# Kernel optimization log

Measured on AMD Instinct MI355X. Metric: run time of the kernel, lower is better.

## Reference

```python
import jax, jax.numpy as jnp
import numpy as np
import math

FEAT_DIM = 256
QUERY_DIM = 256
HIDDEN = 64
OUT_DIM = 256
HEADS = 8


def setup_inputs() -> dict:
    key = jax.random.key(0)
    ks = jax.random.split(key, 10)
    B, NQ, NKV = 2, 2048, 2048
    s_q = 1.0 / math.sqrt(QUERY_DIM)
    s_f = 1.0 / math.sqrt(FEAT_DIM)
    s_o = 1.0 / math.sqrt(HIDDEN * HEADS)
    return {
        "feat": jax.random.normal(ks[0], (B, NKV, FEAT_DIM), jnp.float32),
        "query": jax.random.normal(ks[1], (B, NQ, QUERY_DIM), jnp.float32),
        # stacked per-head weights (each head has its own Linear in torch)
        "Wq": jax.random.uniform(ks[2], (HEADS, QUERY_DIM, HIDDEN), jnp.float32, -s_q, s_q),
        "bq": jax.random.uniform(ks[3], (HEADS, HIDDEN), jnp.float32, -s_q, s_q),
        "Wk": jax.random.uniform(ks[4], (HEADS, FEAT_DIM, HIDDEN), jnp.float32, -s_f, s_f),
        "bk": jax.random.uniform(ks[5], (HEADS, HIDDEN), jnp.float32, -s_f, s_f),
        "Wv": jax.random.uniform(ks[6], (HEADS, FEAT_DIM, HIDDEN), jnp.float32, -s_f, s_f),
        "bv": jax.random.uniform(ks[7], (HEADS, HIDDEN), jnp.float32, -s_f, s_f),
        "Wo": jax.random.uniform(ks[8], (HEADS * HIDDEN, OUT_DIM), jnp.float32, -s_o, s_o),
        "bo": jax.random.uniform(ks[9], (OUT_DIM,), jnp.float32, -s_o, s_o),
    }


def reference(feat, query, Wq, bq, Wk, bk, Wv, bv, Wo, bo):
    # Per-head projections, vectorized over the head axis h.
    # q: [B, H, Nq, E]; k, v: [B, H, Nkv, E]
    q = jnp.einsum("bnd,hde->bhne", query, Wq) + bq[None, :, None, :]
    k = jnp.einsum("bnd,hde->bhne", feat, Wk) + bk[None, :, None, :]
    v = jnp.einsum("bnd,hde->bhne", feat, Wv) + bv[None, :, None, :]
    scale = 1.0 / math.sqrt(HIDDEN)
    scores = jnp.einsum("bhqe,bhke->bhqk", q, k) * scale  # [B, H, Nq, Nkv]
    prob = jax.nn.softmax(scores, axis=-1)
    # dropout p=0.0 (eval) -> identity
    heads = jnp.einsum("bhqk,bhke->bhqe", prob, v)  # [B, H, Nq, E]
    # concat heads in order (head 0 first) then output projection
    B, H, NQ, E = heads.shape
    cat = heads.transpose(0, 2, 1, 3).reshape(B, NQ, H * E)
    return cat @ Wo + bo
```

## Files before the change

kernel.cpp:

```cpp
#include <hip/hip_runtime.h>
#include <hip/hip_bf16.h>

typedef unsigned short u16;
typedef __attribute__((ext_vector_type(8))) short short8;
typedef __attribute__((ext_vector_type(4))) float f32x4;
typedef __attribute__((ext_vector_type(16))) float f32x16;
typedef __attribute__((ext_vector_type(2))) int v2i;

#define HEADS 8
#define HID 64
#define QSCALE 0.18033688011112042f

__device__ inline u16 f2bf(float f){
    unsigned u = __float_as_uint(f);
    unsigned r = (u + 0x7fffu + ((u >> 16) & 1u)) >> 16;
    return (u16)r;
}

__device__ inline int cvtpk(float lo, float hi){
    int r;
    asm("v_cvt_pk_bf16_f32 %0, %1, %2" : "=v"(r) : "v"(lo), "v"(hi));
    return r;
}

__device__ inline float exp2fast(float x){
    float r;
    asm("v_exp_f32 %0, %1" : "=v"(r) : "v"(x));
    return r;
}

__device__ inline float xhalf_sum(float x){
    v2i r = __builtin_amdgcn_permlane32_swap(__float_as_int(x), __float_as_int(x), false, false);
    return __int_as_float(r.x) + __int_as_float(r.y);
}

__global__ __launch_bounds__(256) void prep_weights(
    const float* __restrict__ query, const float* __restrict__ feat,
    const float* __restrict__ Wq, const float* __restrict__ Wk,
    const float* __restrict__ Wv, const float* __restrict__ Wo,
    u16* __restrict__ Xbq, u16* __restrict__ Xbf,
    u16* __restrict__ WfT, u16* __restrict__ WoT)
{
    int id = blockIdx.x * 256 + threadIdx.x;
    if (id < 262144) {
        const float* src = (id < 131072) ? query : feat;
        u16* dst = (id < 131072) ? Xbq : Xbf;
        int r = (id < 131072) ? id : id - 131072;
        int row = r >> 5;
        int rb = row >> 5, r5 = row & 31;
        int ks = (r & 31) >> 1, hi = r & 1;
        float4 a = *reinterpret_cast<const float4*>(&src[r * 8]);
        float4 b = *reinterpret_cast<const float4*>(&src[r * 8 + 4]);
        uint4 s;
        s.x = (unsigned)cvtpk(a.x, a.y);
        s.y = (unsigned)cvtpk(a.z, a.w);
        s.z = (unsigned)cvtpk(b.x, b.y);
        s.w = (unsigned)cvtpk(b.z, b.w);
        *reinterpret_cast<uint4*>(&dst[((rb * 16 + ks) * 64 + hi * 32 + r5) * 8]) = s;
    } else if (id < 655360) {
        int id2 = id - 262144;
        int w = id2 / 131072;
        int r = id2 % 131072;
        int c = r >> 8;
        int d = r & 255;
        const float* W = (w == 0) ? Wq : (w == 1 ? Wk : Wv);
        size_t idx = (size_t)(((w * 16 + (c >> 5)) * 16 + (d >> 4)) * 64
                              + ((d >> 3) & 1) * 32 + (c & 31)) * 8 + (d & 7);
        WfT[idx] = f2bf(W[(c >> 6) * (256 * 64) + d * 64 + (c & 63)]);
    } else {
        int r = id - 655360;
        int o = r >> 9;
        int k = r & 511;
        WoT[o * 512 + k] = f2bf(Wo[k * 256 + o]);
    }
}

__global__ __launch_bounds__(256, 2) void proj_kernel(
    const u16* __restrict__ Xbq, const u16* __restrict__ Xbf,
    const u16* __restrict__ WfT,
    const float* __restrict__ bq, const float* __restrict__ bk, const float* __restrict__ bv,
    u16* __restrict__ Qb, u16* __restrict__ KVf)
{
    int lb = blockIdx.x;
    int which = lb % 3;
    int rem = lb / 3;
    int rb = rem & 127;
    int nh = rem >> 7;
    const u16* Xb = (which == 0) ? Xbq : Xbf;
    const float* bias = (which == 0) ? bq : (which == 1 ? bk : bv);

    int t = threadIdx.x, lane = t & 63, w = t >> 6;
    int l31 = lane & 31, hh = lane >> 5;

    __shared__ __align__(16) u16 Xl[8192];

    {
        const u16* gsrc = Xb + (size_t)rb * 8192;
        #pragma unroll
        for (int c = 0; c < 4; c++) {
            int off = (w * 4 + c) * 512 + lane * 8;
            __builtin_amdgcn_global_load_lds(
                (const __attribute__((address_space(1))) unsigned int*)(const void*)(gsrc + off),
                (__attribute__((address_space(3))) unsigned int*)(void*)(Xl + off),
                16, 0, 0);
        }
    }
    asm volatile("s_waitcnt vmcnt(0)" ::: "memory");
    __syncthreads();

    int nb0 = nh * 8 + w * 2;
    const u16* W0 = WfT + (size_t)(which * 16 + nb0) * 8192 + lane * 8;
    const u16* W1 = W0 + 8192;

    f32x16 acc0 = {}, acc1 = {};
    #pragma unroll
    for (int ks = 0; ks < 16; ks++) {
        short8 xf = *reinterpret_cast<const short8*>(Xl + ks * 512 + lane * 8);
        short8 w0 = *reinterpret_cast<const short8*>(W0 + ks * 512);
        short8 w1 = *reinterpret_cast<const short8*>(W1 + ks * 512);
        if (which == 2) {
            acc0 = __builtin_amdgcn_mfma_f32_32x32x16_bf16(xf, w0, acc0, 0, 0, 0);
            acc1 = __builtin_amdgcn_mfma_f32_32x32x16_bf16(xf, w1, acc1, 0, 0, 0);
        } else {
            acc0 = __builtin_amdgcn_mfma_f32_32x32x16_bf16(w0, xf, acc0, 0, 0, 0);
            acc1 = __builtin_amdgcn_mfma_f32_32x32x16_bf16(w1, xf, acc1, 0, 0, 0);
        }
    }

    int h = nh * 4 + w;
    int nbase = nh * 256 + w * 64;

    if (which != 2) {
        int m = rb * 32 + l31;
        int b_ = m >> 11, nq = m & 2047;
        int bh = b_ * 8 + h;
        int tile = nq >> 6, nl = nq & 63;
        #pragma unroll
        for (int f = 0; f < 2; f++) {
            const f32x16& A = f ? acc1 : acc0;
            #pragma unroll
            for (int g = 0; g < 4; g++) {
                int e0 = f * 32 + g * 8 + 4 * hh;
                float4 b4 = *reinterpret_cast<const float4*>(&bias[nbase + e0]);
                float v0 = A[4*g+0] + b4.x, v1 = A[4*g+1] + b4.y;
                float v2 = A[4*g+2] + b4.z, v3 = A[4*g+3] + b4.w;
                v2i st;
                if (which == 0) {
                    st.x = cvtpk(v0 * QSCALE, v1 * QSCALE);
                    st.y = cvtpk(v2 * QSCALE, v3 * QSCALE);
                    *reinterpret_cast<v2i*>(&Qb[(size_t)(bh * 2048 + nq) * 64 + e0]) = st;
                } else {
                    st.x = cvtpk(v0, v1);
                    st.y = cvtpk(v2, v3);
                    int regK = ((nl >> 5) << 2) | (e0 >> 4);
                    int lnK  = (nl & 31) | (((e0 >> 3) & 1) << 5);
                    size_t idx = (size_t)(bh * 32 + tile) * 8192 + regK * 512 + lnK * 8 + (e0 & 7);
                    *reinterpret_cast<v2i*>(&KVf[idx]) = st;
                }
            }
        }
    } else {
        #pragma unroll
        for (int f = 0; f < 2; f++) {
            const f32x16& A = f ? acc1 : acc0;
            int n_g = nbase + f * 32 + l31;
            int e = n_g & 63;
            float bscal = bias[n_g];
            #pragma unroll
            for (int g = 0; g < 4; g++) {
                int kvl = g * 8 + 4 * hh;
                int m = rb * 32 + kvl;
                int b_ = m >> 11, nkv = m & 2047;
                int tile = nkv >> 6, nl = nkv & 63;
                int bh = b_ * 8 + h;
                float v0 = A[4*g+0] + bscal, v1 = A[4*g+1] + bscal;
                float v2 = A[4*g+2] + bscal, v3 = A[4*g+3] + bscal;
                v2i st;
                st.x = cvtpk(v0, v1);
                st.y = cvtpk(v2, v3);
                int regV = ((e >> 5) << 2) | (nl >> 4);
                int lnV  = (e & 31) | (((nl >> 3) & 1) << 5);
                size_t idx = (size_t)(bh * 32 + tile) * 8192 + 4096 + regV * 512 + lnV * 8 + (nl & 7);
                *reinterpret_cast<v2i*>(&KVf[idx]) = st;
            }
        }
    }
}

__global__ __launch_bounds__(512, 2) void attn_kernel(
    const u16* __restrict__ Qb, const u16* __restrict__ KVf, u16* __restrict__ cat)
{
    int lb = blockIdx.x;
    int chunk = lb >> 4;
    int bh = ((lb & 7) << 1) | ((lb >> 3) & 1);
    int b_ = bh >> 3, head = bh & 7;
    int t = threadIdx.x, lane = t & 63, w = t >> 6;
    int l31 = lane & 31, hh = lane >> 5;
    int sp = w >> 1, kvh = w & 1, wi = w >> 1;
    int q0 = chunk * 128 + sp * 32;

    __shared__ __align__(16) u16 smem[34304];
    u16* tiles = smem;
    float* Ol = (float*)smem;
    float* Ll = (float*)((char*)smem + 67584);

    const u16* KVfB = KVf + ((size_t)(bh * 32 + kvh * 16)) * 8192;

    short8 qf[4];
    {
        const u16* qp = Qb + (bh * 2048 + q0 + l31) * 64 + hh * 8;
        #pragma unroll
        for (int kc = 0; kc < 4; kc++)
            qf[kc] = *reinterpret_cast<const short8*>(qp + kc * 16);
    }
    asm volatile("s_waitcnt vmcnt(0)" ::: "memory");

#define PACKP(sb, base, out) {                                              \
        int A0 = cvtpk(sb[base+0], sb[base+1]);                             \
        int B0 = cvtpk(sb[base+4], sb[base+5]);                             \
        v2i r0 = __builtin_amdgcn_permlane32_swap(A0, B0, false, false);    \
        int A1 = cvtpk(sb[base+2], sb[base+3]);                             \
        int B1 = cvtpk(sb[base+6], sb[base+7]);                             \
        v2i r1 = __builtin_amdgcn_permlane32_swap(A1, B1, false, false);    \
        union { int i[4]; short8 s; } uu;                                   \
        uu.i[0] = r0.x; uu.i[1] = r1.x; uu.i[2] = r0.y; uu.i[3] = r1.y;     \
        out = uu.s; }

    auto stage = [&](int buf, int tile) {
        const u16* gsrc = KVfB + (size_t)tile * 8192;
        u16* ldst = tiles + (kvh * 2 + buf) * 8192;
        #pragma unroll
        for (int c = 0; c < 4; c++) {
            int off = (wi * 4 + c) * 512 + lane * 8;
            __builtin_amdgcn_global_load_lds(
                (const __attribute__((address_space(1))) unsigned int*)(const void*)(gsrc + off),
                (__attribute__((address_space(3))) unsigned int*)(void*)(ldst + off),
                16, 0, 0);
        }
    };

    f32x16 o0 = {}, o1 = {};
    float ac0 = 0.f, ac1 = 0.f, ac2 = 0.f, ac3 = 0.f;

    stage(0, 0);
    int cur = 0;
    for (int tt = 0; tt < 16; tt++) {
        if (tt < 15) {
            stage(cur ^ 1, tt + 1);
            asm volatile("s_waitcnt vmcnt(4)" ::: "memory");
        } else {
            asm volatile("s_waitcnt vmcnt(0)" ::: "memory");
        }
        __builtin_amdgcn_s_barrier();
        __builtin_amdgcn_sched_barrier(0);

        const u16* kbase = tiles + (kvh * 2 + cur) * 8192;
        short8 kf[8], vf[8];
        #pragma unroll
        for (int r = 0; r < 8; r++)
            kf[r] = *reinterpret_cast<const short8*>(kbase + r * 512 + lane * 8);
        #pragma unroll
        for (int r = 0; r < 8; r++)
            vf[r] = *reinterpret_cast<const short8*>(kbase + 4096 + r * 512 + lane * 8);

        f32x16 s0 = {}, s1 = {};
        #pragma unroll
        for (int kc = 0; kc < 4; kc++)
            s0 = __builtin_amdgcn_mfma_f32_32x32x16_bf16(kf[kc], qf[kc], s0, 0, 0, 0);
        #pragma unroll
        for (int kc = 0; kc < 4; kc++)
            s1 = __builtin_amdgcn_mfma_f32_32x32x16_bf16(kf[4 + kc], qf[kc], s1, 0, 0, 0);

        #pragma unroll
        for (int r = 0; r < 16; r++) {
            float p0 = exp2fast(s0[r]);
            float p1 = exp2fast(s1[r]);
            s0[r] = p0; s1[r] = p1;
            if ((r & 3) == 0) ac0 += p0 + p1;
            else if ((r & 3) == 1) ac1 += p0 + p1;
            else if ((r & 3) == 2) ac2 += p0 + p1;
            else ac3 += p0 + p1;
        }

        short8 pf[4];
        PACKP(s0, 0, pf[0]); PACKP(s0, 8, pf[1]);
        PACKP(s1, 0, pf[2]); PACKP(s1, 8, pf[3]);

        #pragma unroll
        for (int c = 0; c < 4; c++) {
            o0 = __builtin_amdgcn_mfma_f32_32x32x16_bf16(vf[c],     pf[c], o0, 0, 0, 0);
            o1 = __builtin_amdgcn_mfma_f32_32x32x16_bf16(vf[4 + c], pf[c], o1, 0, 0, 0);
        }

        asm volatile("s_waitcnt lgkmcnt(0)" ::: "memory");
        __builtin_amdgcn_s_barrier();
        __builtin_amdgcn_sched_barrier(0);
        cur ^= 1;
    }

    float lrun = xhalf_sum((ac0 + ac1) + (ac2 + ac3));

    #pragma unroll
    for (int eb = 0; eb < 2; eb++) {
        #pragma unroll
        for (int r = 0; r < 16; r++) {
            int d = eb * 32 + (r & 3) + 8 * (r >> 2) + 4 * hh;
            Ol[(w * 64 + d) * 33 + l31] = eb ? o1[r] : o0[r];
        }
    }
    if (hh == 0) Ll[w * 32 + l31] = lrun;
    __syncthreads();

    {
        int msp = t >> 7;
        int tt2 = t & 127;
        int q = tt2 >> 2;
        int d0 = (tt2 & 3) * 16;
        int wA = msp * 2, wB = msp * 2 + 1;
        float lsum = Ll[wA * 32 + q] + Ll[wB * 32 + q];
        float linv = 1.0f / lsum;
        float vv[16];
        #pragma unroll
        for (int j = 0; j < 16; j++)
            vv[j] = (Ol[(wA * 64 + d0 + j) * 33 + q] +
                     Ol[(wB * 64 + d0 + j) * 33 + q]) * linv;
        uint4 st0, st1;
        st0.x = (unsigned)cvtpk(vv[0],  vv[1]);
        st0.y = (unsigned)cvtpk(vv[2],  vv[3]);
        st0.z = (unsigned)cvtpk(vv[4],  vv[5]);
        st0.w = (unsigned)cvtpk(vv[6],  vv[7]);
        st1.x = (unsigned)cvtpk(vv[8],  vv[9]);
        st1.y = (unsigned)cvtpk(vv[10], vv[11]);
        st1.z = (unsigned)cvtpk(vv[12], vv[13]);
        st1.w = (unsigned)cvtpk(vv[14], vv[15]);
        u16* crow = cat + (b_ * 2048 + chunk * 128 + msp * 32 + q) * 512 + head * 64 + d0;
        *reinterpret_cast<uint4*>(crow) = st0;
        *reinterpret_cast<uint4*>(crow + 8) = st1;
    }
#undef PACKP
}

__global__ __launch_bounds__(256) void outproj_kernel(
    const u16* __restrict__ cat, const u16* __restrict__ WoT,
    const float* __restrict__ bo, float* __restrict__ out)
{
    int m0 = blockIdx.x * 64, n0 = blockIdx.y * 64;
    int t = threadIdx.x, lane = t & 63, w = t >> 6;
    int l15 = lane & 15, kof = (lane >> 4) * 8;

    __shared__ __align__(16) u16 lA[64][72];
    __shared__ __align__(16) u16 lB[64][72];

    f32x4 acc[4] = {};
    for (int kt = 0; kt < 512; kt += 64) {
        #pragma unroll
        for (int i = 0; i < 2; i++) {
            int lin = t + i * 256;
            int row = lin >> 3, c8 = (lin & 7) * 8;
            *reinterpret_cast<uint4*>(&lA[row][c8]) =
                *reinterpret_cast<const uint4*>(&cat[(m0 + row) * 512 + kt + c8]);
            *reinterpret_cast<uint4*>(&lB[row][c8]) =
                *reinterpret_cast<const uint4*>(&WoT[(n0 + row) * 512 + kt + c8]);
        }
        __syncthreads();
        #pragma unroll
        for (int ks = 0; ks < 2; ks++) {
            short8 a = *reinterpret_cast<const short8*>(&lA[w * 16 + l15][ks * 32 + kof]);
            #pragma unroll
            for (int nt = 0; nt < 4; nt++) {
                short8 b = *reinterpret_cast<const short8*>(&lB[nt * 16 + l15][ks * 32 + kof]);
                acc[nt] = __builtin_amdgcn_mfma_f32_16x16x32_bf16(a, b, acc[nt], 0, 0, 0);
            }
        }
        __syncthreads();
    }
    #pragma unroll
    for (int i = 0; i < 4; i++) {
        int mrow = m0 + w * 16 + (lane >> 4) * 4 + i;
        #pragma unroll
        for (int nt = 0; nt < 4; nt++) {
            int col = n0 + nt * 16 + l15;
            out[mrow * 256 + col] = acc[nt][i] + bo[col];
        }
    }
}

extern "C" void kernel_launch(void* const* d_in, const int* in_sizes, int n_in,
                              void* d_out, int out_size, void* d_ws, size_t ws_size,
                              hipStream_t stream) {
    const float* feat  = (const float*)d_in[0];
    const float* query = (const float*)d_in[1];
    const float* Wq = (const float*)d_in[2];
    const float* bq = (const float*)d_in[3];
    const float* Wk = (const float*)d_in[4];
    const float* bk = (const float*)d_in[5];
    const float* Wv = (const float*)d_in[6];
    const float* bv = (const float*)d_in[7];
    const float* Wo = (const float*)d_in[8];
    const float* bo = (const float*)d_in[9];
    float* out = (float*)d_out;

    char* ws = (char*)d_ws;
    u16* WfT = (u16*)(ws + 0);
    u16* WoT = (u16*)(ws + 786432);
    u16* Qb  = (u16*)(ws + 1048576);
    u16* KVf = (u16*)(ws + 5242880);
    u16* cat = (u16*)(ws + 13631488);
    u16* Xbq = (u16*)(ws + 17825792);
    u16* Xbf = (u16*)(ws + 19922944);

    hipLaunchKernelGGL(prep_weights, dim3(3072), dim3(256), 0, stream,
                       query, feat, Wq, Wk, Wv, Wo, Xbq, Xbf, WfT, WoT);
    hipLaunchKernelGGL(proj_kernel, dim3(768), dim3(256), 0, stream,
                       Xbq, Xbf, WfT, bq, bk, bv, Qb, KVf);
    hipLaunchKernelGGL(attn_kernel, dim3(256), dim3(512), 0, stream,
                       Qb, KVf, cat);
    hipLaunchKernelGGL(outproj_kernel, dim3(64, 4), dim3(256), 0, stream,
                       cat, WoT, bo, out);
}
```

Before: 51.22 us.

## Process two query sub-tiles per wave in attention to reuse K/V fragments

Halves the attention block to 256 threads (4 waves), with each wave now handling 64 queries as two 32-row sub-tiles that share the same K and V fragments loaded from LDS. Each wave stages twice as many global-to-LDS loads per tile, and the final reduction and store layout are remapped to the new slot arrangement. The intent is to halve LDS fragment reads per query and raise MFMA work per wave. In exchange, per-wave register pressure roughly doubles for accumulators, there are fewer waves per CU to hide latency, and the launch-bounds hint limiting occupancy is removed.

```diff
diff --git a/kernel.cpp b/kernel.cpp
--- a/kernel.cpp
+++ b/kernel.cpp
@@ -187,7 +187,7 @@
     }
 }
 
-__global__ __launch_bounds__(512, 2) void attn_kernel(
+__global__ __launch_bounds__(256) void attn_kernel(
     const u16* __restrict__ Qb, const u16* __restrict__ KVf, u16* __restrict__ cat)
 {
     int lb = blockIdx.x;
@@ -196,8 +196,8 @@
     int b_ = bh >> 3, head = bh & 7;
     int t = threadIdx.x, lane = t & 63, w = t >> 6;
     int l31 = lane & 31, hh = lane >> 5;
-    int sp = w >> 1, kvh = w & 1, wi = w >> 1;
-    int q0 = chunk * 128 + sp * 32;
+    int sp = w >> 1, kvh = w & 1;
+    int q0 = chunk * 128 + sp * 64;
 
     __shared__ __align__(16) u16 smem[34304];
     u16* tiles = smem;
@@ -206,12 +206,14 @@
 
     const u16* KVfB = KVf + ((size_t)(bh * 32 + kvh * 16)) * 8192;
 
-    short8 qf[4];
+    short8 qfA[4], qfB[4];
     {
         const u16* qp = Qb + (bh * 2048 + q0 + l31) * 64 + hh * 8;
         #pragma unroll
-        for (int kc = 0; kc < 4; kc++)
-            qf[kc] = *reinterpret_cast<const short8*>(qp + kc * 16);
+        for (int kc = 0; kc < 4; kc++) {
+            qfA[kc] = *reinterpret_cast<const short8*>(qp + kc * 16);
+            qfB[kc] = *reinterpret_cast<const short8*>(qp + 32 * 64 + kc * 16);
+        }
     }
     asm volatile("s_waitcnt vmcnt(0)" ::: "memory");
 
@@ -230,8 +232,8 @@
         const u16* gsrc = KVfB + (size_t)tile * 8192;
         u16* ldst = tiles + (kvh * 2 + buf) * 8192;
         #pragma unroll
-        for (int c = 0; c < 4; c++) {
-            int off = (wi * 4 + c) * 512 + lane * 8;
+        for (int c = 0; c < 8; c++) {
+            int off = (sp * 8 + c) * 512 + lane * 8;
             __builtin_amdgcn_global_load_lds(
                 (const __attribute__((address_space(1))) unsigned int*)(const void*)(gsrc + off),
                 (__attribute__((address_space(3))) unsigned int*)(void*)(ldst + off),
@@ -239,15 +241,16 @@
         }
     };
 
-    f32x16 o0 = {}, o1 = {};
-    float ac0 = 0.f, ac1 = 0.f, ac2 = 0.f, ac3 = 0.f;
+    f32x16 oA0 = {}, oA1 = {}, oB0 = {}, oB1 = {};
+    float aA0 = 0.f, aA1 = 0.f, aA2 = 0.f, aA3 = 0.f;
+    float aB0 = 0.f, aB1 = 0.f, aB2 = 0.f, aB3 = 0.f;
 
     stage(0, 0);
     int cur = 0;
     for (int tt = 0; tt < 16; tt++) {
         if (tt < 15) {
             stage(cur ^ 1, tt + 1);
-            asm volatile("s_waitcnt vmcnt(4)" ::: "memory");
+            asm volatile("s_waitcnt vmcnt(8)" ::: "memory");
         } else {
             asm volatile("s_waitcnt vmcnt(0)" ::: "memory");
         }
@@ -263,33 +266,59 @@
         for (int r = 0; r < 8; r++)
             vf[r] = *reinterpret_cast<const short8*>(kbase + 4096 + r * 512 + lane * 8);
 
-        f32x16 s0 = {}, s1 = {};
-        #pragma unroll
-        for (int kc = 0; kc < 4; kc++)
-            s0 = __builtin_amdgcn_mfma_f32_32x32x16_bf16(kf[kc], qf[kc], s0, 0, 0, 0);
-        #pragma unroll
-        for (int kc = 0; kc < 4; kc++)
-            s1 = __builtin_amdgcn_mfma_f32_32x32x16_bf16(kf[4 + kc], qf[kc], s1, 0, 0, 0);
-
-        #pragma unroll
-        for (int r = 0; r < 16; r++) {
-            float p0 = exp2fast(s0[r]);
-            float p1 = exp2fast(s1[r]);
-            s0[r] = p0; s1[r] = p1;
-            if ((r & 3) == 0) ac0 += p0 + p1;
-            else if ((r & 3) == 1) ac1 += p0 + p1;
-            else if ((r & 3) == 2) ac2 += p0 + p1;
-            else ac3 += p0 + p1;
-        }
-
-        short8 pf[4];
-        PACKP(s0, 0, pf[0]); PACKP(s0, 8, pf[1]);
-        PACKP(s1, 0, pf[2]); PACKP(s1, 8, pf[3]);
-
-        #pragma unroll
-        for (int c = 0; c < 4; c++) {
-            o0 = __builtin_amdgcn_mfma_f32_32x32x16_bf16(vf[c],     pf[c], o0, 0, 0, 0);
-            o1 = __builtin_amdgcn_mfma_f32_32x32x16_bf16(vf[4 + c], pf[c], o1, 0, 0, 0);
+        {
+            f32x16 s0 = {}, s1 = {};
+            #pragma unroll
+            for (int kc = 0; kc < 4; kc++)
+                s0 = __builtin_amdgcn_mfma_f32_32x32x16_bf16(kf[kc], qfA[kc], s0, 0, 0, 0);
+            #pragma unroll
+            for (int kc = 0; kc < 4; kc++)
+                s1 = __builtin_amdgcn_mfma_f32_32x32x16_bf16(kf[4 + kc], qfA[kc], s1, 0, 0, 0);
+            #pragma unroll
+            for (int r = 0; r < 16; r++) {
+                float p0 = exp2fast(s0[r]);
+                float p1 = exp2fast(s1[r]);
+                s0[r] = p0; s1[r] = p1;
+                if ((r & 3) == 0) aA0 += p0 + p1;
+                else if ((r & 3) == 1) aA1 += p0 + p1;
+                else if ((r & 3) == 2) aA2 += p0 + p1;
+                else aA3 += p0 + p1;
+            }
+            short8 pf[4];
+            PACKP(s0, 0, pf[0]); PACKP(s0, 8, pf[1]);
+            PACKP(s1, 0, pf[2]); PACKP(s1, 8, pf[3]);
+            #pragma unroll
+            for (int c = 0; c < 4; c++) {
+                oA0 = __builtin_amdgcn_mfma_f32_32x32x16_bf16(vf[c],     pf[c], oA0, 0, 0, 0);
+                oA1 = __builtin_amdgcn_mfma_f32_32x32x16_bf16(vf[4 + c], pf[c], oA1, 0, 0, 0);
+            }
+        }
+        {
+            f32x16 s0 = {}, s1 = {};
+            #pragma unroll
+            for (int kc = 0; kc < 4; kc++)
+                s0 = __builtin_amdgcn_mfma_f32_32x32x16_bf16(kf[kc], qfB[kc], s0, 0, 0, 0);
+            #pragma unroll
+            for (int kc = 0; kc < 4; kc++)
+                s1 = __builtin_amdgcn_mfma_f32_32x32x16_bf16(kf[4 + kc], qfB[kc], s1, 0, 0, 0);
+            #pragma unroll
+            for (int r = 0; r < 16; r++) {
+                float p0 = exp2fast(s0[r]);
+                float p1 = exp2fast(s1[r]);
+                s0[r] = p0; s1[r] = p1;
+                if ((r & 3) == 0) aB0 += p0 + p1;
+                else if ((r & 3) == 1) aB1 += p0 + p1;
+                else if ((r & 3) == 2) aB2 += p0 + p1;
+                else aB3 += p0 + p1;
+            }
+            short8 pf[4];
+            PACKP(s0, 0, pf[0]); PACKP(s0, 8, pf[1]);
+            PACKP(s1, 0, pf[2]); PACKP(s1, 8, pf[3]);
+            #pragma unroll
+            for (int c = 0; c < 4; c++) {
+                oB0 = __builtin_amdgcn_mfma_f32_32x32x16_bf16(vf[c],     pf[c], oB0, 0, 0, 0);
+                oB1 = __builtin_amdgcn_mfma_f32_32x32x16_bf16(vf[4 + c], pf[c], oB1, 0, 0, 0);
+            }
         }
 
         asm volatile("s_waitcnt lgkmcnt(0)" ::: "memory");
@@ -298,44 +327,47 @@
         cur ^= 1;
     }
 
-    float lrun = xhalf_sum((ac0 + ac1) + (ac2 + ac3));
-
+    float lA = xhalf_sum((aA0 + aA1) + (aA2 + aA3));
+    float lB = xhalf_sum((aB0 + aB1) + (aB2 + aB3));
+
+    int slotA = sp * 4 + kvh;
+    int slotB = sp * 4 + 2 + kvh;
     #pragma unroll
     for (int eb = 0; eb < 2; eb++) {
         #pragma unroll
         for (int r = 0; r < 16; r++) {
             int d = eb * 32 + (r & 3) + 8 * (r >> 2) + 4 * hh;
-            Ol[(w * 64 + d) * 33 + l31] = eb ? o1[r] : o0[r];
-        }
-    }
-    if (hh == 0) Ll[w * 32 + l31] = lrun;
+            Ol[(slotA * 64 + d) * 33 + l31] = eb ? oA1[r] : oA0[r];
+            Ol[(slotB * 64 + d) * 33 + l31] = eb ? oB1[r] : oB0[r];
+        }
+    }
+    if (hh == 0) { Ll[slotA * 32 + l31] = lA; Ll[slotB * 32 + l31] = lB; }
     __syncthreads();
 
     {
-        int msp = t >> 7;
-        int tt2 = t & 127;
-        int q = tt2 >> 2;
-        int d0 = (tt2 & 3) * 16;
-        int wA = msp * 2, wB = msp * 2 + 1;
-        float lsum = Ll[wA * 32 + q] + Ll[wB * 32 + q];
+        int g = t >> 6;
+        int tt2 = t & 63;
+        int q = tt2 >> 1;
+        int dh = (tt2 & 1) * 32;
+        int sA = g * 2, sB = g * 2 + 1;
+        float lsum = Ll[sA * 32 + q] + Ll[sB * 32 + q];
         float linv = 1.0f / lsum;
-        float vv[16];
-        #pragma unroll
-        for (int j = 0; j < 16; j++)
-            vv[j] = (Ol[(wA * 64 + d0 + j) * 33 + q] +
-                     Ol[(wB * 64 + d0 + j) * 33 + q]) * linv;
-        uint4 st0, st1;
-        st0.x = (unsigned)cvtpk(vv[0],  vv[1]);
-        st0.y = (unsigned)cvtpk(vv[2],  vv[3]);
-        st0.z = (unsigned)cvtpk(vv[4],  vv[5]);
-        st0.w = (unsigned)cvtpk(vv[6],  vv[7]);
-        st1.x = (unsigned)cvtpk(vv[8],  vv[9]);
-        st1.y = (unsigned)cvtpk(vv[10], vv[11]);
-        st1.z = (unsigned)cvtpk(vv[12], vv[13]);
-        st1.w = (unsigned)cvtpk(vv[14], vv[15]);
-        u16* crow = cat + (b_ * 2048 + chunk * 128 + msp * 32 + q) * 512 + head * 64 + d0;
-        *reinterpret_cast<uint4*>(crow) = st0;
-        *reinterpret_cast<uint4*>(crow + 8) = st1;
+        float vv[32];
+        #pragma unroll
+        for (int j = 0; j < 32; j++)
+            vv[j] = (Ol[(sA * 64 + dh + j) * 33 + q] +
+                     Ol[(sB * 64 + dh + j) * 33 + q]) * linv;
+        int row = b_ * 2048 + chunk * 128 + g * 32 + q;
+        u16* crow = cat + row * 512 + head * 64 + dh;
+        #pragma unroll
+        for (int k = 0; k < 4; k++) {
+            uint4 st;
+            st.x = (unsigned)cvtpk(vv[8*k+0], vv[8*k+1]);
+            st.y = (unsigned)cvtpk(vv[8*k+2], vv[8*k+3]);
+            st.z = (unsigned)cvtpk(vv[8*k+4], vv[8*k+5]);
+            st.w = (unsigned)cvtpk(vv[8*k+6], vv[8*k+7]);
+            *reinterpret_cast<uint4*>(crow + k * 8) = st;
+        }
     }
 #undef PACKP
 }
@@ -413,7 +445,7 @@
                        query, feat, Wq, Wk, Wv, Wo, Xbq, Xbf, WfT, WoT);
     hipLaunchKernelGGL(proj_kernel, dim3(768), dim3(256), 0, stream,
                        Xbq, Xbf, WfT, bq, bk, bv, Qb, KVf);
-    hipLaunchKernelGGL(attn_kernel, dim3(256), dim3(512), 0, stream,
+    hipLaunchKernelGGL(attn_kernel, dim3(256), dim3(256), 0, stream,
                        Qb, KVf, cat);
     hipLaunchKernelGGL(outproj_kernel, dim3(64, 4), dim3(256), 0, stream,
                        cat, WoT, bo, out);
```

After: 54.40 us. 6.2% more time.
